# Kernel tuning notes

Hardware: AMD Instinct MI355X
Metric: run time of the kernel (lower is better)

The kernel has to match this reference:

```python
import jax, jax.numpy as jnp
import numpy as np

N = 2_000_000  # hits
D = 4          # track-parameter dim
P = 50_000     # number of particle ids (0 = noise)


def setup_inputs() -> dict:
    key = jax.random.key(0)
    k1, k2, k3, k4, k5 = jax.random.split(key, 5)
    # beta in (0, 1) open interval so arctanh stays finite
    beta = jax.random.uniform(k1, (N,), jnp.float32, 0.01, 0.99)
    pred = jax.random.normal(k2, (N, D), jnp.float32)
    track_params = jax.random.normal(k3, (N, D), jnp.float32)
    particle_id = jax.random.randint(k4, (N,), 0, P)
    reconstructable = jax.random.randint(k5, (N,), 0, 2)
    return {
        "beta": beta,
        "pred": pred,
        "particle_id": particle_id,
        "track_params": track_params,
        "reconstructable": reconstructable,
    }


def reference(beta, pred, particle_id, track_params, reconstructable):
    # mask = reconstructable > 0; instead of gathering a dynamic subset,
    # route masked-out hits (and pid==0 noise) to segment 0, which is dropped.
    valid = reconstructable > 0
    seg = jnp.where(valid, particle_id, 0)

    # per-hit squared-error summed over parameter dim (mse_loss reduction='none' then sum(dim=1))
    mse = jnp.sum((pred - track_params) ** 2, axis=1)  # [N]
    xi = jnp.arctanh(beta) ** 2                         # [N]

    # segmented replacement of the dense N x P pid_masks broadcast:
    # terms_p = sum_i mse_i * xi_i * [pid_i == p], xi_p_norm_p = sum_i xi_i * [pid_i == p]
    num = jax.ops.segment_sum(mse * xi, seg, num_segments=P)  # [P]
    den = jax.ops.segment_sum(xi, seg, num_segments=P)        # [P]

    # mean over real particle ids 1..P-1 (segment 0 holds noise + masked hits)
    return jnp.mean(num[1:] / den[1:])
```

## Files before the change

### kernel.cpp

```cpp
#include <hip/hip_runtime.h>
#include <stdint.h>

#define P_IDS   50000
#define NBUCK   32
#define BUCK_W  1563
#define HPT     8
#define BLK_HITS (256 * HPT)
#define M_PER   64
#define SUBB    16


__global__ void __launch_bounds__(256)
phaseA_bucket(const float* __restrict__ beta,
              const float4* __restrict__ pred,
              const int* __restrict__ pid_arr,
              const float4* __restrict__ track,
              const int* __restrict__ recon,
              int* __restrict__ cnt_arr,
              uint2* __restrict__ recs,
              float* __restrict__ out,
              int n, int nblk) {
    __shared__ uint2 stage[NBUCK * M_PER];
    __shared__ int cursor[NBUCK];
    __shared__ int prefx[NBUCK];
    const int t = threadIdx.x;
    if (t < NBUCK) cursor[t] = 0;
    if (blockIdx.x == 0 && t == 0) *out = 0.0f;
    __syncthreads();

    const int B = blockIdx.x * BLK_HITS;

    int    p_[HPT], r_[HPT];
    float  b_[HPT];
    float4 pr_[HPT], tp_[HPT];
    #pragma unroll
    for (int h = 0; h < HPT; ++h) {
        int i = B + h * 256 + t;
        if (i < n) {
            p_[h]  = pid_arr[i];
            r_[h]  = recon[i];
            b_[h]  = beta[i];
            pr_[h] = pred[i];
            tp_[h] = track[i];
        } else {
            p_[h] = 0; r_[h] = 0; b_[h] = 0.5f;
            pr_[h] = make_float4(0.f,0.f,0.f,0.f);
            tp_[h] = make_float4(0.f,0.f,0.f,0.f);
        }
    }

    #pragma unroll
    for (int h = 0; h < HPT; ++h) {
        int p = p_[h], r = r_[h];
        if (r > 0 && p > 0) {
            float4 pr = pr_[h], tp = tp_[h];
            float dx = pr.x - tp.x, dy = pr.y - tp.y;
            float dz = pr.z - tp.z, dw = pr.w - tp.w;
            float mse = dx*dx + dy*dy + dz*dz + dw*dw;
            float at = 0.5f * logf((1.0f + b_[h]) / (1.0f - b_[h]));
            float xi = at * at;
            int bb = p / BUCK_W;
            int pl = p - bb * BUCK_W;
            int rank = atomicAdd(&cursor[bb], 1);
            if (rank < M_PER) {
                uint2 rr;
                rr.x = (__float_as_uint(xi) & 0xFFFFF800u) | (uint32_t)pl;
                rr.y = __float_as_uint(mse * xi);
                stage[bb * M_PER + rank] = rr;
            }
        }
    }
    __syncthreads();

    if (t < 64) {
        int c = (t < NBUCK) ? min(cursor[t], M_PER) : 0;
        int x = c;
        #pragma unroll
        for (int d = 1; d < NBUCK; d <<= 1) {
            int y = __shfl_up(x, d, 64);
            if (t >= d) x += y;
        }
        if (t < NBUCK) {
            int excl = x - c;
            prefx[t] = excl;
            cnt_arr[blockIdx.x * NBUCK + t] = (excl << 16) | c;
        }
    }
    __syncthreads();

    uint2* dst = recs + (size_t)blockIdx.x * (NBUCK * M_PER);
    #pragma unroll
    for (int k = 0; k < 8; ++k) {
        int slot = t + k * 256;
        int bb = slot >> 6, rank = slot & 63;
        if (rank < min(cursor[bb], M_PER))
            dst[prefx[bb] + rank] = stage[slot];
    }
}

__global__ void __launch_bounds__(256)
phaseB_bin(const int* __restrict__ cnt_arr,
           const uint2* __restrict__ recs,
           float2* __restrict__ partials,
           int nblk) {
    __shared__ float2 hist[BUCK_W];
    int part = blockIdx.x / SUBB;
    int sub  = blockIdx.x % SUBB;

    for (int j = threadIdx.x; j < BUCK_W; j += 256)
        hist[j] = make_float2(0.0f, 0.0f);
    __syncthreads();

    int lane  = threadIdx.x & 63;
    int half  = lane >> 5;
    int hlane = lane & 31;
    int wid   = threadIdx.x >> 6;
    int wslot = sub * 4 + wid;
    const int nslots = SUBB * 4;

    for (int bp = wslot * 2; bp < nblk; bp += nslots * 2) {
        int b = bp + half;
        if (b < nblk) {
            int pc  = cnt_arr[b * NBUCK + part];
            int off = pc >> 16, cnt = pc & 0xFFFF;
            const uint2* r = recs + (size_t)b * (NBUCK * M_PER) + off;
            for (int idx = hlane; idx < cnt; idx += 32) {
                uint2 rr = r[idx];
                int   pl  = rr.x & 0x7FFu;
                float xi  = __uint_as_float(rr.x & 0xFFFFF800u);
                float num = __uint_as_float(rr.y);
                atomicAdd(&hist[pl].x, num);
                atomicAdd(&hist[pl].y, xi);
            }
        }
    }
    __syncthreads();

    float2* dst = partials + (size_t)blockIdx.x * BUCK_W;
    for (int j = threadIdx.x; j < BUCK_W; j += 256)
        dst[j] = hist[j];
}

__global__ void __launch_bounds__(256)
phaseC_mean(const float2* __restrict__ partials,
            float* __restrict__ out) {
    double local = 0.0;
    int stride = gridDim.x * blockDim.x;
    for (int p = 1 + blockIdx.x * blockDim.x + threadIdx.x; p < P_IDS; p += stride) {
        int part = p / BUCK_W;
        int loc  = p % BUCK_W;
        const float2* base = partials + ((size_t)part * SUBB) * BUCK_W + loc;
        float num = 0.0f, den = 0.0f;
        #pragma unroll
        for (int s = 0; s < SUBB; ++s) {
            float2 v = base[(size_t)s * BUCK_W];
            num += v.x;
            den += v.y;
        }
        local += (double)(num / den);
    }

    for (int off = 32; off > 0; off >>= 1)
        local += __shfl_down(local, off, 64);

    __shared__ double wave_sums[4];
    int lane = threadIdx.x & 63;
    int wid  = threadIdx.x >> 6;
    if (lane == 0) wave_sums[wid] = local;
    __syncthreads();

    if (threadIdx.x == 0) {
        double s = wave_sums[0] + wave_sums[1] + wave_sums[2] + wave_sums[3];
        atomicAdd(out, (float)(s / (double)(P_IDS - 1)));
    }
}

__global__ void __launch_bounds__(256)
scatter_fallback(const float* __restrict__ beta,
                 const float4* __restrict__ pred,
                 const int* __restrict__ pid,
                 const float4* __restrict__ track,
                 const int* __restrict__ recon,
                 float2* __restrict__ bins, int n) {
    int i = blockIdx.x * blockDim.x + threadIdx.x;
    if (i >= n) return;
    int p = pid[i];
    int r = recon[i];
    if (r <= 0 || p <= 0) return;
    float  b  = beta[i];
    float4 pr = pred[i];
    float4 tp = track[i];
    float dx = pr.x - tp.x, dy = pr.y - tp.y, dz = pr.z - tp.z, dw = pr.w - tp.w;
    float mse = dx*dx + dy*dy + dz*dz + dw*dw;
    float at = 0.5f * logf((1.0f + b) / (1.0f - b));
    float xi = at * at;
    atomicAdd(&bins[p].x, mse * xi);
    atomicAdd(&bins[p].y, xi);
}

__global__ void __launch_bounds__(256)
reduce_fallback(const float2* __restrict__ bins, float* __restrict__ out) {
    double local = 0.0;
    int stride = gridDim.x * blockDim.x;
    for (int p = 1 + blockIdx.x * blockDim.x + threadIdx.x; p < P_IDS; p += stride) {
        float2 v = bins[p];
        local += (double)(v.x / v.y);
    }
    for (int off = 32; off > 0; off >>= 1)
        local += __shfl_down(local, off, 64);
    __shared__ double wave_sums[4];
    int lane = threadIdx.x & 63;
    int wid  = threadIdx.x >> 6;
    if (lane == 0) wave_sums[wid] = local;
    __syncthreads();
    if (threadIdx.x == 0) {
        double s = wave_sums[0] + wave_sums[1] + wave_sums[2] + wave_sums[3];
        atomicAdd(out, (float)(s / (double)(P_IDS - 1)));
    }
}

extern "C" void kernel_launch(void* const* d_in, const int* in_sizes, int n_in,
                              void* d_out, int out_size, void* d_ws, size_t ws_size,
                              hipStream_t stream) {
    const float*  beta  = (const float*)d_in[0];
    const float4* pred  = (const float4*)d_in[1];
    const int*    pid   = (const int*)d_in[2];
    const float4* track = (const float4*)d_in[3];
    const int*    recon = (const int*)d_in[4];
    float* out = (float*)d_out;
    int n = in_sizes[0];

    int nblk = (n + BLK_HITS - 1) / BLK_HITS;

    size_t recs_bytes = sizeof(uint2) * (size_t)nblk * NBUCK * M_PER;
    size_t recs_pad   = (recs_bytes + 255) & ~(size_t)255;
    size_t cnt_bytes  = sizeof(int) * (size_t)nblk * NBUCK;
    size_t cnt_pad    = (cnt_bytes + 255) & ~(size_t)255;
    size_t part_bytes = sizeof(float2) * (size_t)NBUCK * SUBB * BUCK_W;
    size_t needed = recs_pad + cnt_pad + part_bytes;

    if (ws_size >= needed) {
        uint2*  recs     = (uint2*)d_ws;
        int*    cnt_arr  = (int*)((char*)d_ws + recs_pad);
        float2* partials = (float2*)((char*)d_ws + recs_pad + cnt_pad);

        phaseA_bucket<<<nblk, 256, 0, stream>>>(beta, pred, pid, track, recon,
                                                cnt_arr, recs, out, n, nblk);
        phaseB_bin<<<NBUCK * SUBB, 256, 0, stream>>>(cnt_arr, recs, partials, nblk);
        phaseC_mean<<<196, 256, 0, stream>>>(partials, out);
    } else {
        float2* bins = (float2*)d_ws;
        hipMemsetAsync(bins, 0, P_IDS * sizeof(float2), stream);
        hipMemsetAsync(d_out, 0, sizeof(float), stream);
        int grid = (n + 255) / 256;
        scatter_fallback<<<grid, 256, 0, stream>>>(beta, pred, pid, track, recon,
                                                   bins, n);
        reduce_fallback<<<196, 256, 0, stream>>>(bins, out);
    }
}
```

Baseline: 130.9 us.

## Replace three-phase bucket sort with direct global float atomics and single-block reduce

Removes the bucketed staging pipeline (per-block LDS staging, record writes to workspace, LDS histogram pass, and partial-sum merge) and instead scatters each valid hit straight into a 50k-entry global bin array using unsafeAtomicAdd, which can map to hardware float atomics. The final mean is computed by one 1024-thread block that writes the output directly instead of atomically accumulating into it. This cuts one kernel launch and the intermediate workspace traffic. In exchange it relies on contended global atomics over about a million hits and adds a memset.

```diff
diff --git a/kernel.cpp b/kernel.cpp
--- a/kernel.cpp
+++ b/kernel.cpp
@@ -2,32 +2,27 @@
 #include <stdint.h>
 
 #define P_IDS   50000
-#define NBUCK   32
-#define BUCK_W  1563
 #define HPT     8
 #define BLK_HITS (256 * HPT)
-#define M_PER   64
-#define SUBB    16
 
 
+__device__ __forceinline__ void fadd_memside(float* p, float v) {
+#if defined(__HIP_PLATFORM_AMD__) || defined(__HIPCC__)
+    unsafeAtomicAdd(p, v);
+#else
+    atomicAdd(p, v);
+#endif
+}
+
 __global__ void __launch_bounds__(256)
-phaseA_bucket(const float* __restrict__ beta,
-              const float4* __restrict__ pred,
-              const int* __restrict__ pid_arr,
-              const float4* __restrict__ track,
-              const int* __restrict__ recon,
-              int* __restrict__ cnt_arr,
-              uint2* __restrict__ recs,
-              float* __restrict__ out,
-              int n, int nblk) {
-    __shared__ uint2 stage[NBUCK * M_PER];
-    __shared__ int cursor[NBUCK];
-    __shared__ int prefx[NBUCK];
+scatter_atomic(const float* __restrict__ beta,
+               const float4* __restrict__ pred,
+               const int* __restrict__ pid_arr,
+               const float4* __restrict__ track,
+               const int* __restrict__ recon,
+               float2* __restrict__ bins,
+               int n) {
     const int t = threadIdx.x;
-    if (t < NBUCK) cursor[t] = 0;
-    if (blockIdx.x == 0 && t == 0) *out = 0.0f;
-    __syncthreads();
-
     const int B = blockIdx.x * BLK_HITS;
 
     int    p_[HPT], r_[HPT];
@@ -44,178 +39,49 @@
             tp_[h] = track[i];
         } else {
             p_[h] = 0; r_[h] = 0; b_[h] = 0.5f;
-            pr_[h] = make_float4(0.f,0.f,0.f,0.f);
-            tp_[h] = make_float4(0.f,0.f,0.f,0.f);
+            pr_[h] = make_float4(0.f, 0.f, 0.f, 0.f);
+            tp_[h] = make_float4(0.f, 0.f, 0.f, 0.f);
         }
     }
 
     #pragma unroll
     for (int h = 0; h < HPT; ++h) {
-        int p = p_[h], r = r_[h];
-        if (r > 0 && p > 0) {
+        int p = p_[h];
+        if (r_[h] > 0 && p > 0) {
             float4 pr = pr_[h], tp = tp_[h];
             float dx = pr.x - tp.x, dy = pr.y - tp.y;
             float dz = pr.z - tp.z, dw = pr.w - tp.w;
             float mse = dx*dx + dy*dy + dz*dz + dw*dw;
             float at = 0.5f * logf((1.0f + b_[h]) / (1.0f - b_[h]));
             float xi = at * at;
-            int bb = p / BUCK_W;
-            int pl = p - bb * BUCK_W;
-            int rank = atomicAdd(&cursor[bb], 1);
-            if (rank < M_PER) {
-                uint2 rr;
-                rr.x = (__float_as_uint(xi) & 0xFFFFF800u) | (uint32_t)pl;
-                rr.y = __float_as_uint(mse * xi);
-                stage[bb * M_PER + rank] = rr;
-            }
+            fadd_memside(&bins[p].x, mse * xi);
+            fadd_memside(&bins[p].y, xi);
         }
-    }
-    __syncthreads();
-
-    if (t < 64) {
-        int c = (t < NBUCK) ? min(cursor[t], M_PER) : 0;
-        int x = c;
-        #pragma unroll
-        for (int d = 1; d < NBUCK; d <<= 1) {
-            int y = __shfl_up(x, d, 64);
-            if (t >= d) x += y;
-        }
-        if (t < NBUCK) {
-            int excl = x - c;
-            prefx[t] = excl;
-            cnt_arr[blockIdx.x * NBUCK + t] = (excl << 16) | c;
-        }
-    }
-    __syncthreads();
-
-    uint2* dst = recs + (size_t)blockIdx.x * (NBUCK * M_PER);
-    #pragma unroll
-    for (int k = 0; k < 8; ++k) {
-        int slot = t + k * 256;
-        int bb = slot >> 6, rank = slot & 63;
-        if (rank < min(cursor[bb], M_PER))
-            dst[prefx[bb] + rank] = stage[slot];
     }
 }
 
-__global__ void __launch_bounds__(256)
-phaseB_bin(const int* __restrict__ cnt_arr,
-           const uint2* __restrict__ recs,
-           float2* __restrict__ partials,
-           int nblk) {
-    __shared__ float2 hist[BUCK_W];
-    int part = blockIdx.x / SUBB;
-    int sub  = blockIdx.x % SUBB;
-
-    for (int j = threadIdx.x; j < BUCK_W; j += 256)
-        hist[j] = make_float2(0.0f, 0.0f);
-    __syncthreads();
-
-    int lane  = threadIdx.x & 63;
-    int half  = lane >> 5;
-    int hlane = lane & 31;
-    int wid   = threadIdx.x >> 6;
-    int wslot = sub * 4 + wid;
-    const int nslots = SUBB * 4;
-
-    for (int bp = wslot * 2; bp < nblk; bp += nslots * 2) {
-        int b = bp + half;
-        if (b < nblk) {
-            int pc  = cnt_arr[b * NBUCK + part];
-            int off = pc >> 16, cnt = pc & 0xFFFF;
-            const uint2* r = recs + (size_t)b * (NBUCK * M_PER) + off;
-            for (int idx = hlane; idx < cnt; idx += 32) {
-                uint2 rr = r[idx];
-                int   pl  = rr.x & 0x7FFu;
-                float xi  = __uint_as_float(rr.x & 0xFFFFF800u);
-                float num = __uint_as_float(rr.y);
-                atomicAdd(&hist[pl].x, num);
-                atomicAdd(&hist[pl].y, xi);
-            }
-        }
-    }
-    __syncthreads();
-
-    float2* dst = partials + (size_t)blockIdx.x * BUCK_W;
-    for (int j = threadIdx.x; j < BUCK_W; j += 256)
-        dst[j] = hist[j];
-}
-
-__global__ void __launch_bounds__(256)
-phaseC_mean(const float2* __restrict__ partials,
-            float* __restrict__ out) {
+__global__ void __launch_bounds__(1024)
+reduce_mean(const float2* __restrict__ bins, float* __restrict__ out) {
     double local = 0.0;
-    int stride = gridDim.x * blockDim.x;
-    for (int p = 1 + blockIdx.x * blockDim.x + threadIdx.x; p < P_IDS; p += stride) {
-        int part = p / BUCK_W;
-        int loc  = p % BUCK_W;
-        const float2* base = partials + ((size_t)part * SUBB) * BUCK_W + loc;
-        float num = 0.0f, den = 0.0f;
-        #pragma unroll
-        for (int s = 0; s < SUBB; ++s) {
-            float2 v = base[(size_t)s * BUCK_W];
-            num += v.x;
-            den += v.y;
-        }
-        local += (double)(num / den);
+    for (int p = 1 + threadIdx.x; p < P_IDS; p += 1024) {
+        float2 v = bins[p];
+        local += (double)(v.x / v.y);
     }
 
     for (int off = 32; off > 0; off >>= 1)
         local += __shfl_down(local, off, 64);
 
-    __shared__ double wave_sums[4];
+    __shared__ double wave_sums[16];
     int lane = threadIdx.x & 63;
     int wid  = threadIdx.x >> 6;
     if (lane == 0) wave_sums[wid] = local;
     __syncthreads();
 
     if (threadIdx.x == 0) {
-        double s = wave_sums[0] + wave_sums[1] + wave_sums[2] + wave_sums[3];
-        atomicAdd(out, (float)(s / (double)(P_IDS - 1)));
-    }
-}
-
-__global__ void __launch_bounds__(256)
-scatter_fallback(const float* __restrict__ beta,
-                 const float4* __restrict__ pred,
-                 const int* __restrict__ pid,
-                 const float4* __restrict__ track,
-                 const int* __restrict__ recon,
-                 float2* __restrict__ bins, int n) {
-    int i = blockIdx.x * blockDim.x + threadIdx.x;
-    if (i >= n) return;
-    int p = pid[i];
-    int r = recon[i];
-    if (r <= 0 || p <= 0) return;
-    float  b  = beta[i];
-    float4 pr = pred[i];
-    float4 tp = track[i];
-    float dx = pr.x - tp.x, dy = pr.y - tp.y, dz = pr.z - tp.z, dw = pr.w - tp.w;
-    float mse = dx*dx + dy*dy + dz*dz + dw*dw;
-    float at = 0.5f * logf((1.0f + b) / (1.0f - b));
-    float xi = at * at;
-    atomicAdd(&bins[p].x, mse * xi);
-    atomicAdd(&bins[p].y, xi);
-}
-
-__global__ void __launch_bounds__(256)
-reduce_fallback(const float2* __restrict__ bins, float* __restrict__ out) {
-    double local = 0.0;
-    int stride = gridDim.x * blockDim.x;
-    for (int p = 1 + blockIdx.x * blockDim.x + threadIdx.x; p < P_IDS; p += stride) {
-        float2 v = bins[p];
-        local += (double)(v.x / v.y);
-    }
-    for (int off = 32; off > 0; off >>= 1)
-        local += __shfl_down(local, off, 64);
-    __shared__ double wave_sums[4];
-    int lane = threadIdx.x & 63;
-    int wid  = threadIdx.x >> 6;
-    if (lane == 0) wave_sums[wid] = local;
-    __syncthreads();
-    if (threadIdx.x == 0) {
-        double s = wave_sums[0] + wave_sums[1] + wave_sums[2] + wave_sums[3];
-        atomicAdd(out, (float)(s / (double)(P_IDS - 1)));
+        double s = 0.0;
+        #pragma unroll
+        for (int w = 0; w < 16; ++w) s += wave_sums[w];
+        out[0] = (float)(s / (double)(P_IDS - 1));
     }
 }
 
@@ -230,31 +96,14 @@
     float* out = (float*)d_out;
     int n = in_sizes[0];
 
+    if (ws_size < P_IDS * sizeof(float2)) return;
+
+    float2* bins = (float2*)d_ws;
+
+    hipMemsetAsync(bins, 0, P_IDS * sizeof(float2), stream);
+
     int nblk = (n + BLK_HITS - 1) / BLK_HITS;
-
-    size_t recs_bytes = sizeof(uint2) * (size_t)nblk * NBUCK * M_PER;
-    size_t recs_pad   = (recs_bytes + 255) & ~(size_t)255;
-    size_t cnt_bytes  = sizeof(int) * (size_t)nblk * NBUCK;
-    size_t cnt_pad    = (cnt_bytes + 255) & ~(size_t)255;
-    size_t part_bytes = sizeof(float2) * (size_t)NBUCK * SUBB * BUCK_W;
-    size_t needed = recs_pad + cnt_pad + part_bytes;
-
-    if (ws_size >= needed) {
-        uint2*  recs     = (uint2*)d_ws;
-        int*    cnt_arr  = (int*)((char*)d_ws + recs_pad);
-        float2* partials = (float2*)((char*)d_ws + recs_pad + cnt_pad);
-
-        phaseA_bucket<<<nblk, 256, 0, stream>>>(beta, pred, pid, track, recon,
-                                                cnt_arr, recs, out, n, nblk);
-        phaseB_bin<<<NBUCK * SUBB, 256, 0, stream>>>(cnt_arr, recs, partials, nblk);
-        phaseC_mean<<<196, 256, 0, stream>>>(partials, out);
-    } else {
-        float2* bins = (float2*)d_ws;
-        hipMemsetAsync(bins, 0, P_IDS * sizeof(float2), stream);
-        hipMemsetAsync(d_out, 0, sizeof(float), stream);
-        int grid = (n + 255) / 256;
-        scatter_fallback<<<grid, 256, 0, stream>>>(beta, pred, pid, track, recon,
-                                                   bins, n);
-        reduce_fallback<<<196, 256, 0, stream>>>(bins, out);
-    }
+    scatter_atomic<<<nblk, 256, 0, stream>>>(beta, pred, pid, track, recon,
+                                             bins, n);
+    reduce_mean<<<1, 1024, 0, stream>>>(bins, out);
 }
```

New measurement: 222.7 us. 70.1% more time.

## Replace per-block record slabs with per-bucket global arenas via atomic cursors

Applied to the files above, without the earlier changes.

Phase A no longer writes per-block bucket slabs with a prefix-sum header. Each block now reserves space in a contiguous per-bucket arena through one global atomicAdd per bucket, then writes its staged records there. Phase B can then stream its bucket's records as one contiguous range split evenly across sub-blocks, instead of walking per-block count headers with short variable-length loops. This costs two memset launches and global atomic contention on 32 counters, and records past the arena capacity would be dropped silently.

```diff
diff --git a/kernel.cpp b/kernel.cpp
--- a/kernel.cpp
+++ b/kernel.cpp
@@ -8,6 +8,7 @@
 #define BLK_HITS (256 * HPT)
 #define M_PER   64
 #define SUBB    16
+#define ARENA_CAP 65536
 
 
 __global__ void __launch_bounds__(256)
@@ -16,16 +17,14 @@
               const int* __restrict__ pid_arr,
               const float4* __restrict__ track,
               const int* __restrict__ recon,
-              int* __restrict__ cnt_arr,
-              uint2* __restrict__ recs,
-              float* __restrict__ out,
-              int n, int nblk) {
+              uint2* __restrict__ arena,
+              int* __restrict__ cursor_g,
+              int n) {
     __shared__ uint2 stage[NBUCK * M_PER];
     __shared__ int cursor[NBUCK];
-    __shared__ int prefx[NBUCK];
+    __shared__ int base_g[NBUCK];
     const int t = threadIdx.x;
     if (t < NBUCK) cursor[t] = 0;
-    if (blockIdx.x == 0 && t == 0) *out = 0.0f;
     __syncthreads();
 
     const int B = blockIdx.x * BLK_HITS;
@@ -51,8 +50,8 @@
 
     #pragma unroll
     for (int h = 0; h < HPT; ++h) {
-        int p = p_[h], r = r_[h];
-        if (r > 0 && p > 0) {
+        int p = p_[h];
+        if (r_[h] > 0 && p > 0) {
             float4 pr = pr_[h], tp = tp_[h];
             float dx = pr.x - tp.x, dy = pr.y - tp.y;
             float dz = pr.z - tp.z, dw = pr.w - tp.w;
@@ -72,37 +71,28 @@
     }
     __syncthreads();
 
-    if (t < 64) {
-        int c = (t < NBUCK) ? min(cursor[t], M_PER) : 0;
-        int x = c;
-        #pragma unroll
-        for (int d = 1; d < NBUCK; d <<= 1) {
-            int y = __shfl_up(x, d, 64);
-            if (t >= d) x += y;
-        }
-        if (t < NBUCK) {
-            int excl = x - c;
-            prefx[t] = excl;
-            cnt_arr[blockIdx.x * NBUCK + t] = (excl << 16) | c;
-        }
-    }
-    __syncthreads();
-
-    uint2* dst = recs + (size_t)blockIdx.x * (NBUCK * M_PER);
+    if (t < NBUCK) {
+        int c = min(cursor[t], M_PER);
+        base_g[t] = atomicAdd(&cursor_g[t], c);
+    }
+    __syncthreads();
+
     #pragma unroll
     for (int k = 0; k < 8; ++k) {
         int slot = t + k * 256;
         int bb = slot >> 6, rank = slot & 63;
-        if (rank < min(cursor[bb], M_PER))
-            dst[prefx[bb] + rank] = stage[slot];
-    }
-}
-
-__global__ void __launch_bounds__(256)
-phaseB_bin(const int* __restrict__ cnt_arr,
-           const uint2* __restrict__ recs,
-           float2* __restrict__ partials,
-           int nblk) {
+        if (rank < min(cursor[bb], M_PER)) {
+            int dst = base_g[bb] + rank;
+            if (dst < ARENA_CAP)
+                arena[(size_t)bb * ARENA_CAP + dst] = stage[slot];
+        }
+    }
+}
+
+__global__ void __launch_bounds__(256)
+phaseB_bin(const uint2* __restrict__ arena,
+           const int* __restrict__ cursor_g,
+           float2* __restrict__ partials) {
     __shared__ float2 hist[BUCK_W];
     int part = blockIdx.x / SUBB;
     int sub  = blockIdx.x % SUBB;
@@ -111,28 +101,16 @@
         hist[j] = make_float2(0.0f, 0.0f);
     __syncthreads();
 
-    int lane  = threadIdx.x & 63;
-    int half  = lane >> 5;
-    int hlane = lane & 31;
-    int wid   = threadIdx.x >> 6;
-    int wslot = sub * 4 + wid;
-    const int nslots = SUBB * 4;
-
-    for (int bp = wslot * 2; bp < nblk; bp += nslots * 2) {
-        int b = bp + half;
-        if (b < nblk) {
-            int pc  = cnt_arr[b * NBUCK + part];
-            int off = pc >> 16, cnt = pc & 0xFFFF;
-            const uint2* r = recs + (size_t)b * (NBUCK * M_PER) + off;
-            for (int idx = hlane; idx < cnt; idx += 32) {
-                uint2 rr = r[idx];
-                int   pl  = rr.x & 0x7FFu;
-                float xi  = __uint_as_float(rr.x & 0xFFFFF800u);
-                float num = __uint_as_float(rr.y);
-                atomicAdd(&hist[pl].x, num);
-                atomicAdd(&hist[pl].y, xi);
-            }
-        }
+    int cnt = min(cursor_g[part], ARENA_CAP);
+    int lo = (int)((long long)cnt * sub / SUBB);
+    int hi = (int)((long long)cnt * (sub + 1) / SUBB);
+    const uint2* __restrict__ r = arena + (size_t)part * ARENA_CAP;
+
+    for (int i = lo + threadIdx.x; i < hi; i += 256) {
+        uint2 rr = r[i];
+        int   pl  = rr.x & 0x7FFu;
+        atomicAdd(&hist[pl].x, __uint_as_float(rr.y));
+        atomicAdd(&hist[pl].y, __uint_as_float(rr.x & 0xFFFFF800u));
     }
     __syncthreads();
 
@@ -230,28 +208,28 @@
     float* out = (float*)d_out;
     int n = in_sizes[0];
 
-    int nblk = (n + BLK_HITS - 1) / BLK_HITS;
-
-    size_t recs_bytes = sizeof(uint2) * (size_t)nblk * NBUCK * M_PER;
-    size_t recs_pad   = (recs_bytes + 255) & ~(size_t)255;
-    size_t cnt_bytes  = sizeof(int) * (size_t)nblk * NBUCK;
-    size_t cnt_pad    = (cnt_bytes + 255) & ~(size_t)255;
-    size_t part_bytes = sizeof(float2) * (size_t)NBUCK * SUBB * BUCK_W;
-    size_t needed = recs_pad + cnt_pad + part_bytes;
+    size_t arena_bytes = sizeof(uint2) * (size_t)NBUCK * ARENA_CAP;
+    size_t cur_pad     = 256;
+    size_t part_bytes  = sizeof(float2) * (size_t)NBUCK * SUBB * BUCK_W;
+    size_t needed = arena_bytes + cur_pad + part_bytes;
 
     if (ws_size >= needed) {
-        uint2*  recs     = (uint2*)d_ws;
-        int*    cnt_arr  = (int*)((char*)d_ws + recs_pad);
-        float2* partials = (float2*)((char*)d_ws + recs_pad + cnt_pad);
-
+        uint2*  arena    = (uint2*)d_ws;
+        int*    cursor_g = (int*)((char*)d_ws + arena_bytes);
+        float2* partials = (float2*)((char*)d_ws + arena_bytes + cur_pad);
+
+        hipMemsetAsync(cursor_g, 0, NBUCK * sizeof(int), stream);
+        hipMemsetAsync(out, 0, sizeof(float), stream);
+
+        int nblk = (n + BLK_HITS - 1) / BLK_HITS;
         phaseA_bucket<<<nblk, 256, 0, stream>>>(beta, pred, pid, track, recon,
-                                                cnt_arr, recs, out, n, nblk);
-        phaseB_bin<<<NBUCK * SUBB, 256, 0, stream>>>(cnt_arr, recs, partials, nblk);
+                                                arena, cursor_g, n);
+        phaseB_bin<<<NBUCK * SUBB, 256, 0, stream>>>(arena, cursor_g, partials);
         phaseC_mean<<<196, 256, 0, stream>>>(partials, out);
     } else {
         float2* bins = (float2*)d_ws;
         hipMemsetAsync(bins, 0, P_IDS * sizeof(float2), stream);
-        hipMemsetAsync(d_out, 0, sizeof(float), stream);
+        hipMemsetAsync(out, 0, sizeof(float), stream);
         int grid = (n + 255) / 256;
         scatter_fallback<<<grid, 256, 0, stream>>>(beta, pred, pid, track, recon,
                                                    bins, n);
```

New measurement: 138.8 us. +6.1%, slower.
